# Performance work log

Measured on AMD Instinct MI355X. Metric: run time of the kernel, lower is better.

## Reference

```python
import jax, jax.numpy as jnp
import numpy as np

N = 50000      # nodes
E = 800000     # edges (before self-loops)
F_IN = 128     # num_node_features
HID = 32       # hidden (per-head dim)
H1 = 4         # heads in conv1
G = 64         # graphs in batch


def setup_inputs() -> dict:
    key = jax.random.key(0)
    ks = jax.random.split(key, 12)
    x = jax.random.normal(ks[0], (N, F_IN), jnp.float32)
    edge_index = jax.random.randint(ks[1], (2, E), 0, N)
    batch = jnp.sort(jax.random.randint(ks[2], (N,), 0, G))
    s = lambda k, shape, fan: jax.random.normal(k, shape, jnp.float32) / np.float32(np.sqrt(fan))
    W1 = s(ks[3], (F_IN, H1 * HID), F_IN)
    att_src1 = s(ks[4], (H1, HID), HID)
    att_dst1 = s(ks[5], (H1, HID), HID)
    b1 = jnp.zeros((H1 * HID,), jnp.float32)
    W2 = s(ks[6], (H1 * HID, HID), H1 * HID)
    att_src2 = s(ks[7], (1, HID), HID)
    att_dst2 = s(ks[8], (1, HID), HID)
    b2 = jnp.zeros((HID,), jnp.float32)
    lin1_w = s(ks[9], (HID, HID // 2), HID)
    lin1_b = jnp.zeros((HID // 2,), jnp.float32)
    lin2_w = s(ks[10], (HID // 2, 1), HID // 2)
    lin2_b = jnp.zeros((1,), jnp.float32)
    return dict(x=x, edge_index=edge_index, batch=batch, W1=W1, att_src1=att_src1,
                att_dst1=att_dst1, b1=b1, W2=W2, att_src2=att_src2, att_dst2=att_dst2,
                b2=b2, lin1_w=lin1_w, lin1_b=lin1_b, lin2_w=lin2_w, lin2_b=lin2_b)


def gat_conv(x, src, dst, W, a_src, a_dst, b, heads, dim):
    # PyG GATConv (eval mode): per-edge attention, segment softmax over dst.
    n = x.shape[0]
    h = (x @ W).reshape(n, heads, dim)                         # [N,H,D]
    alpha_src = (h * a_src).sum(-1)                            # [N,H]
    alpha_dst = (h * a_dst).sum(-1)                            # [N,H]
    alpha = jax.nn.leaky_relu(alpha_src[src] + alpha_dst[dst], 0.2)  # [Etot,H]
    amax = jax.ops.segment_max(alpha, dst, num_segments=n)
    e = jnp.exp(alpha - amax[dst])
    denom = jax.ops.segment_sum(e, dst, num_segments=n)
    coef = e / (denom[dst] + 1e-16)
    out = jax.ops.segment_sum(h[src] * coef[:, :, None], dst, num_segments=n)
    return out.reshape(n, heads * dim) + b                     # concat=True


def reference(x, edge_index, batch, W1, att_src1, att_dst1, b1, W2, att_src2,
              att_dst2, b2, lin1_w, lin1_b, lin2_w, lin2_b):
    n = x.shape[0]
    loops = jnp.arange(n, dtype=edge_index.dtype)              # add_self_loops=True
    src = jnp.concatenate([edge_index[0], loops])
    dst = jnp.concatenate([edge_index[1], loops])
    h = jax.nn.elu(gat_conv(x, src, dst, W1, att_src1, att_dst1, b1, H1, HID))
    h = gat_conv(h, src, dst, W2, att_src2, att_dst2, b2, 1, HID)
    counts = jax.ops.segment_sum(jnp.ones((n,), h.dtype), batch, num_segments=G)
    g = jax.ops.segment_sum(h, batch, num_segments=G) / jnp.maximum(counts, 1.0)[:, None]
    g = jax.nn.elu(g @ lin1_w + lin1_b)
    return g @ lin2_w + lin2_b                                  # [G,1]
```

## Files before the change

### kernel.cpp

```cpp
#include <hip/hip_runtime.h>
#include <math.h>

#define N_NODES 50000
#define N_EDGES 800000
#define ETOT (N_EDGES + N_NODES)
#define NG 64
#define NBUCK 196
#define CHUNK 4096
#define NCHUNK ((ETOT + CHUNK - 1)/CHUNK)
#define SCANN (NBUCK*NCHUNK)
#define GSB ((SCANN + 255)/256)

typedef float vf2 __attribute__((ext_vector_type(2)));
typedef short bf16x8 __attribute__((ext_vector_type(8)));
typedef float f32x4 __attribute__((ext_vector_type(4)));

__device__ __forceinline__ float leaky02(float a){ return a > 0.f ? a : 0.2f*a; }
__device__ __forceinline__ float eluf(float v){ return v > 0.f ? v : expm1f(v); }

__device__ __forceinline__ unsigned pack_bf16(float a, float b){
  unsigned ua = __float_as_uint(a); ua += 0x7fffu + ((ua >> 16) & 1u);
  unsigned ub = __float_as_uint(b); ub += 0x7fffu + ((ub >> 16) & 1u);
  return (ua >> 16) | (ub & 0xffff0000u);
}
__device__ __forceinline__ float bf_lo(unsigned v){ return __uint_as_float(v << 16); }
__device__ __forceinline__ float bf_hi(unsigned v){ return __uint_as_float(v & 0xffff0000u); }

__device__ __forceinline__ unsigned pack_fp8x4(float4 a){
  int v = __builtin_amdgcn_cvt_pk_fp8_f32(a.x, a.y, 0, false);
  v = __builtin_amdgcn_cvt_pk_fp8_f32(a.z, a.w, v, true);
  return (unsigned)v;
}

__global__ __launch_bounds__(256) void k_hist(const int* __restrict__ ei,
    unsigned* __restrict__ cnt, const float* __restrict__ W1, const float* __restrict__ W2,
    unsigned* __restrict__ wt1, unsigned* __restrict__ wt2){
  if (blockIdx.x >= NCHUNK){
    int b = blockIdx.x - NCHUNK;
    int t = threadIdx.x;
    if (t < 64){
      if (b < 128){
        float a = W1[(size_t)(2*t)*128 + b];
        float c = W1[(size_t)(2*t+1)*128 + b];
        wt1[b*64 + t] = pack_bf16(a, c);
      } else {
        int cc = b - 128;
        float a = W2[(size_t)(2*t)*32 + cc];
        float c = W2[(size_t)(2*t+1)*32 + cc];
        wt2[cc*64 + t] = pack_bf16(a, c);
      }
    }
    return;
  }
  __shared__ unsigned hist[NBUCK];
  int tid = threadIdx.x;
  for (int t = tid; t < NBUCK; t += 256) hist[t] = 0;
  __syncthreads();
  int base = blockIdx.x * CHUNK;
  #pragma unroll
  for (int i = 0; i < CHUNK/256; ++i){
    int e = base + i*256 + tid;
    if (e < ETOT){
      int d = (e < N_EDGES) ? ei[N_EDGES + e] : (e - N_EDGES);
      atomicAdd(&hist[d >> 8], 1u);
    }
  }
  __syncthreads();
  for (int t = tid; t < NBUCK; t += 256) cnt[t*NCHUNK + blockIdx.x] = hist[t];
}

__global__ __launch_bounds__(256) void g_scan1(const unsigned* __restrict__ in,
    unsigned* __restrict__ bsum, int n){
  int i = blockIdx.x*256 + threadIdx.x;
  unsigned v = (i < n) ? in[i] : 0u;
  #pragma unroll
  for (int o = 32; o >= 1; o >>= 1) v += __shfl_xor(v, o);
  __shared__ unsigned ws[4];
  if ((threadIdx.x & 63) == 0) ws[threadIdx.x >> 6] = v;
  __syncthreads();
  if (threadIdx.x == 0) bsum[blockIdx.x] = ws[0] + ws[1] + ws[2] + ws[3];
}

__global__ __launch_bounds__(256) void g_scan3b(const unsigned* __restrict__ in,
    const unsigned* __restrict__ bsum, unsigned* __restrict__ out, int n){
  __shared__ unsigned bs[256];
  __shared__ unsigned ts[256];
  int t = threadIdx.x, i = blockIdx.x*256 + t;
  bs[t] = (t < GSB && t < blockIdx.x) ? bsum[t] : 0u;
  unsigned v = (i < n) ? in[i] : 0u;
  ts[t] = v;
  __syncthreads();
  #pragma unroll
  for (int o = 128; o >= 1; o >>= 1){
    if (t < o) bs[t] += bs[t + o];
    __syncthreads();
  }
  unsigned base = bs[0];
  for (int o = 1; o < 256; o <<= 1){
    unsigned u = (t >= o) ? ts[t-o] : 0u;
    __syncthreads();
    ts[t] += u;
    __syncthreads();
  }
  if (i < n) out[i] = base + ts[t] - v;
}

__global__ __launch_bounds__(256) void k_part(const int* __restrict__ ei,
    const unsigned* __restrict__ basev, unsigned* __restrict__ staging){
  __shared__ unsigned cur[NBUCK];
  int tid = threadIdx.x;
  for (int t = tid; t < NBUCK; t += 256) cur[t] = basev[t*NCHUNK + blockIdx.x];
  __syncthreads();
  int base = blockIdx.x * CHUNK;
  #pragma unroll
  for (int i = 0; i < CHUNK/256; ++i){
    int e = base + i*256 + tid;
    if (e < ETOT){
      int s, d;
      if (e < N_EDGES){ s = ei[e]; d = ei[N_EDGES + e]; } else { s = d = e - N_EDGES; }
      unsigned pos = atomicAdd(&cur[d >> 8], 1u);
      staging[pos] = (unsigned)s | ((unsigned)(d & 255) << 16);
    }
  }
}

__global__ __launch_bounds__(256) void k_csr(const unsigned* __restrict__ basev,
    const unsigned* __restrict__ staging, unsigned* __restrict__ off,
    int* __restrict__ csr_src){
  __shared__ unsigned ts[256], cur[256];
  int tid = threadIdx.x, b = blockIdx.x;
  unsigned start = basev[b*NCHUNK];
  unsigned end = (b == NBUCK-1) ? (unsigned)ETOT : basev[(b+1)*NCHUNK];
  ts[tid] = 0;
  __syncthreads();
  for (unsigned i = start + tid; i < end; i += 256)
    atomicAdd(&ts[staging[i] >> 16], 1u);
  __syncthreads();
  unsigned v = ts[tid];
  for (int o = 1; o < 256; o <<= 1){
    unsigned u = (tid >= o) ? ts[tid-o] : 0u;
    __syncthreads();
    ts[tid] += u;
    __syncthreads();
  }
  unsigned excl = ts[tid] - v;
  int node = (b << 8) + tid;
  if (node < N_NODES) off[node] = start + excl;
  if (b == 0 && tid == 0) off[N_NODES] = (unsigned)ETOT;
  cur[tid] = excl;
  __syncthreads();
  for (unsigned i = start + tid; i < end; i += 256){
    unsigned p = staging[i];
    unsigned pos = atomicAdd(&cur[p >> 16], 1u);
    csr_src[start + pos] = (int)(p & 0xffffu);
  }
}

__global__ __launch_bounds__(256) void k_gemm1(const float* __restrict__ x,
    const unsigned* __restrict__ wt1, const float* __restrict__ attS,
    const float* __restrict__ attD, unsigned* __restrict__ h1f,
    float* __restrict__ asrc, float* __restrict__ adst)
{
  __shared__ __align__(16) short xs[64*136];
  __shared__ __align__(16) short wb[128*136];
  float* Cst = (float*)wb;
  int tid = threadIdx.x;
  int base = blockIdx.x * 64;
  {
    int row = tid >> 2, q = tid & 3;
    const float* src = x + (size_t)(base + row)*128 + q*32;
    bool valid = (base + row) < N_NODES;
    #pragma unroll
    for (int i = 0; i < 8; ++i){
      float4 v = valid ? *(const float4*)(src + 4*i) : make_float4(0,0,0,0);
      *(uint2*)(&xs[row*136 + q*32 + 4*i]) = make_uint2(pack_bf16(v.x, v.y), pack_bf16(v.z, v.w));
    }
  }
  {
    int c = tid >> 1, h = tid & 1;
    #pragma unroll
    for (int i = 0; i < 8; ++i){
      uint4 v = *(const uint4*)(wt1 + c*64 + h*32 + 4*i);
      *(uint4*)(&wb[c*136 + h*64 + 8*i]) = v;
    }
  }
  __syncthreads();
  int lane = tid & 63, wid = tid >> 6;
  int r = lane & 15, g = lane >> 4;
  bf16x8 afr[4];
  #pragma unroll
  for (int kk = 0; kk < 4; ++kk)
    afr[kk] = *(const bf16x8*)(&xs[(wid*16 + r)*136 + kk*32 + g*8]);
  f32x4 acc[8];
  #pragma unroll
  for (int ct = 0; ct < 8; ++ct){ acc[ct][0]=0.f; acc[ct][1]=0.f; acc[ct][2]=0.f; acc[ct][3]=0.f; }
  #pragma unroll
  for (int ct = 0; ct < 8; ++ct){
    #pragma unroll
    for (int kk = 0; kk < 4; ++kk){
      bf16x8 bfr = *(const bf16x8*)(&wb[(ct*16 + r)*136 + kk*32 + g*8]);
      acc[ct] = __builtin_amdgcn_mfma_f32_16x16x32_bf16(afr[kk], bfr, acc[ct], 0, 0, 0);
    }
  }
  __syncthreads();
  #pragma unroll
  for (int ct = 0; ct < 8; ++ct){
    #pragma unroll
    for (int q = 0; q < 4; ++q)
      Cst[(wid*16 + 4*g + q)*132 + ct*16 + r] = acc[ct][q];
  }
  __syncthreads();
  {
    int row = tid >> 2, hd = tid & 3;
    int grow = base + row;
    if (grow < N_NODES){
      const float* cp = &Cst[row*132 + hd*32];
      const float* aS = attS + hd*32;
      const float* aD = attD + hd*32;
      float ps = 0.f, pd = 0.f;
      unsigned u[8];
      #pragma unroll
      for (int i = 0; i < 8; ++i){
        float4 c4 = *(const float4*)(cp + 4*i);
        ps += c4.x*aS[4*i] + c4.y*aS[4*i+1] + c4.z*aS[4*i+2] + c4.w*aS[4*i+3];
        pd += c4.x*aD[4*i] + c4.y*aD[4*i+1] + c4.z*aD[4*i+2] + c4.w*aD[4*i+3];
        u[i] = pack_fp8x4(c4);
      }
      unsigned* dst = h1f + (size_t)grow*32 + hd*8;
      *(uint4*)(dst)     = make_uint4(u[0], u[1], u[2], u[3]);
      *(uint4*)(dst + 4) = make_uint4(u[4], u[5], u[6], u[7]);
      asrc[grow*4 + hd] = ps;
      adst[grow*4 + hd] = pd;
    }
  }
}

__global__ __launch_bounds__(256) void k_conv1(const unsigned* __restrict__ off,
    const int* __restrict__ csr_src, const unsigned* __restrict__ h1f,
    const float* __restrict__ asrc, const float* __restrict__ adst,
    const float* __restrict__ b1, unsigned* __restrict__ helu_b)
{
  __shared__ uint2 st[4][4][66];
  int w    = threadIdx.x >> 6;
  int lane = threadIdx.x & 63;
  int n = blockIdx.x*4 + w;
  if (n >= N_NODES) return;
  unsigned s0 = off[n];
  int deg = (int)(off[n+1] - s0);
  float4 ad = *(const float4*)(adst + (size_t)n*4);
  int cl = lane & 31;
  int h  = cl >> 3;
  const char* hbase = (const char*)h1f + 4*cl;
  float4 acc = make_float4(0,0,0,0);
  float den = 0.f;

  if (deg <= 64){
    unsigned boff = 0;
    float e0=0.f, e1=0.f, e2=0.f, e3=0.f;
    if (lane < deg){
      int idx = csr_src[s0 + lane];
      boff = ((unsigned)idx) << 7;
      float4 as = *(const float4*)(asrc + (size_t)idx*4);
      e0 = __expf(leaky02(as.x + ad.x));
      e1 = __expf(leaky02(as.y + ad.y));
      e2 = __expf(leaky02(as.z + ad.z));
      e3 = __expf(leaky02(as.w + ad.w));
    }
    st[w][0][lane] = make_uint2(__float_as_uint(e0), boff);
    st[w][1][lane] = make_uint2(__float_as_uint(e1), boff);
    st[w][2][lane] = make_uint2(__float_as_uint(e2), boff);
    st[w][3][lane] = make_uint2(__float_as_uint(e3), boff);
    __builtin_amdgcn_wave_barrier();
    int half = lane >> 5;
    const uint2* sp = &st[w][h][half];
    #pragma unroll 8
    for (int i = 0; i < deg; i += 2){
      uint2 p = sp[i];
      float es = __uint_as_float(p.x);
      unsigned hb = *(const unsigned*)(hbase + p.y);
      vf2 p0 = __builtin_amdgcn_cvt_pk_f32_fp8((int)hb, false);
      vf2 p1 = __builtin_amdgcn_cvt_pk_f32_fp8((int)hb, true);
      acc.x += es*p0[0]; acc.y += es*p0[1];
      acc.z += es*p1[0]; acc.w += es*p1[1];
      den += es;
    }
    acc.x += __shfl_xor(acc.x, 32); acc.y += __shfl_xor(acc.y, 32);
    acc.z += __shfl_xor(acc.z, 32); acc.w += __shfl_xor(acc.w, 32);
    den   += __shfl_xor(den, 32);
  } else {
    float adh = (h==0) ? ad.x : (h==1) ? ad.y : (h==2) ? ad.z : ad.w;
    for (int i = 0; i < deg; ++i){
      int s = csr_src[s0 + i];
      float ev = __expf(leaky02(asrc[s*4 + h] + adh));
      unsigned hb = *(const unsigned*)(hbase + (((unsigned)s) << 7));
      vf2 p0 = __builtin_amdgcn_cvt_pk_f32_fp8((int)hb, false);
      vf2 p1 = __builtin_amdgcn_cvt_pk_f32_fp8((int)hb, true);
      acc.x += ev*p0[0]; acc.y += ev*p0[1];
      acc.z += ev*p1[0]; acc.w += ev*p1[1];
      den += ev;
    }
  }
  if (lane < 32){
    float inv = 1.f/(den + 1e-16f);
    float4 bv = ((const float4*)b1)[cl];
    float ox = eluf(acc.x*inv + bv.x), oy = eluf(acc.y*inv + bv.y);
    float oz = eluf(acc.z*inv + bv.z), ow = eluf(acc.w*inv + bv.w);
    *(uint2*)(helu_b + (size_t)n*64 + 2*cl) = make_uint2(pack_bf16(ox, oy), pack_bf16(oz, ow));
  }
}

__global__ __launch_bounds__(256) void k_gemm2(const unsigned* __restrict__ helu_b,
    const unsigned* __restrict__ wt2, const float* __restrict__ attS,
    const float* __restrict__ attD, unsigned* __restrict__ h2b,
    float* __restrict__ asrc, float* __restrict__ adst)
{
  __shared__ __align__(16) short xs[64*136];
  __shared__ __align__(16) float cbuf[64*36];
  short* w2 = (short*)cbuf;
  int tid = threadIdx.x;
  int base = blockIdx.x * 64;
  {
    int row = tid >> 2, q = tid & 3;
    bool valid = (base + row) < N_NODES;
    const unsigned* src = helu_b + (size_t)(base + row)*64 + q*16;
    #pragma unroll
    for (int i = 0; i < 4; ++i){
      uint4 v = valid ? *(const uint4*)(src + 4*i) : make_uint4(0,0,0,0);
      *(uint4*)(&xs[row*136 + q*32 + 8*i]) = v;
    }
  }
  {
    int c = tid >> 3, h = tid & 7;
    uint4 v0 = *(const uint4*)(wt2 + c*64 + h*8);
    uint4 v1 = *(const uint4*)(wt2 + c*64 + h*8 + 4);
    *(uint4*)(&w2[c*136 + h*16])     = v0;
    *(uint4*)(&w2[c*136 + h*16 + 8]) = v1;
  }
  __syncthreads();
  int lane = tid & 63, wid = tid >> 6;
  int r = lane & 15, g = lane >> 4;
  bf16x8 afr[4];
  #pragma unroll
  for (int kk = 0; kk < 4; ++kk)
    afr[kk] = *(const bf16x8*)(&xs[(wid*16 + r)*136 + kk*32 + g*8]);
  f32x4 acc[2];
  #pragma unroll
  for (int ct = 0; ct < 2; ++ct){ acc[ct][0]=0.f; acc[ct][1]=0.f; acc[ct][2]=0.f; acc[ct][3]=0.f; }
  #pragma unroll
  for (int ct = 0; ct < 2; ++ct){
    #pragma unroll
    for (int kk = 0; kk < 4; ++kk){
      bf16x8 bfr = *(const bf16x8*)(&w2[(ct*16 + r)*136 + kk*32 + g*8]);
      acc[ct] = __builtin_amdgcn_mfma_f32_16x16x32_bf16(afr[kk], bfr, acc[ct], 0, 0, 0);
    }
  }
  __syncthreads();
  #pragma unroll
  for (int ct = 0; ct < 2; ++ct){
    #pragma unroll
    for (int q = 0; q < 4; ++q)
      cbuf[(wid*16 + 4*g + q)*36 + ct*16 + r] = acc[ct][q];
  }
  __syncthreads();
  {
    int row = tid >> 2, q = tid & 3;
    int grow = base + row;
    if (grow < N_NODES){
      const float* cp = &cbuf[row*36 + q*8];
      float4 c0 = *(const float4*)(cp);
      float4 c1 = *(const float4*)(cp + 4);
      *(uint4*)(h2b + (size_t)grow*16 + q*4) =
        make_uint4(pack_bf16(c0.x,c0.y), pack_bf16(c0.z,c0.w),
                   pack_bf16(c1.x,c1.y), pack_bf16(c1.z,c1.w));
    }
  }
  if (tid < 64){
    int grow = base + tid;
    if (grow < N_NODES){
      const float* cp = &cbuf[tid*36];
      float ps = 0.f, pd = 0.f;
      #pragma unroll
      for (int i = 0; i < 8; ++i){
        float4 c4 = *(const float4*)(cp + 4*i);
        ps += c4.x*attS[4*i] + c4.y*attS[4*i+1] + c4.z*attS[4*i+2] + c4.w*attS[4*i+3];
        pd += c4.x*attD[4*i] + c4.y*attD[4*i+1] + c4.z*attD[4*i+2] + c4.w*attD[4*i+3];
      }
      asrc[grow] = ps; adst[grow] = pd;
    }
  }
}

__global__ __launch_bounds__(256) void k_conv2(const unsigned* __restrict__ off,
    const int* __restrict__ csr_src, const unsigned* __restrict__ h2b,
    const float* __restrict__ asrc, const float* __restrict__ adst,
    const float* __restrict__ b2, float* __restrict__ hout)
{
  __shared__ uint2 st[4][66];
  int w    = threadIdx.x >> 6;
  int lane = threadIdx.x & 63;
  int n = blockIdx.x*4 + w;
  if (n >= N_NODES) return;
  unsigned s0 = off[n];
  int deg = (int)(off[n+1] - s0);
  float ad = adst[n];
  int cl = lane & 7;
  const char* hbase = (const char*)h2b + 8*cl;
  float4 acc = make_float4(0,0,0,0);
  float den = 0.f;

  if (deg <= 64){
    unsigned boff = 0;
    float e = 0.f;
    if (lane < deg){
      int idx = csr_src[s0 + lane];
      boff = ((unsigned)idx) << 6;
      e = __expf(leaky02(asrc[idx] + ad));
    }
    st[w][lane] = make_uint2(__float_as_uint(e), boff);
    __builtin_amdgcn_wave_barrier();
    int g8 = lane >> 3;
    const uint2* sp = &st[w][g8];
    #pragma unroll 4
    for (int i = 0; i < deg; i += 8){
      uint2 p = sp[i];
      float es = __uint_as_float(p.x);
      uint2 hb = *(const uint2*)(hbase + p.y);
      acc.x += es*bf_lo(hb.x); acc.y += es*bf_hi(hb.x);
      acc.z += es*bf_lo(hb.y); acc.w += es*bf_hi(hb.y);
      den += es;
    }
    #pragma unroll
    for (int mm = 8; mm <= 32; mm <<= 1){
      acc.x += __shfl_xor(acc.x, mm); acc.y += __shfl_xor(acc.y, mm);
      acc.z += __shfl_xor(acc.z, mm); acc.w += __shfl_xor(acc.w, mm);
      den   += __shfl_xor(den, mm);
    }
  } else {
    for (int i = 0; i < deg; ++i){
      int s = csr_src[s0 + i];
      float ev = __expf(leaky02(asrc[s] + ad));
      uint2 hb = *(const uint2*)(hbase + (((unsigned)s) << 6));
      acc.x += ev*bf_lo(hb.x); acc.y += ev*bf_hi(hb.x);
      acc.z += ev*bf_lo(hb.y); acc.w += ev*bf_hi(hb.y);
      den += ev;
    }
  }
  if (lane < 8){
    float inv = 1.f/(den + 1e-16f);
    float4 bv = ((const float4*)b2)[cl];
    float4 o;
    o.x = acc.x*inv + bv.x; o.y = acc.y*inv + bv.y;
    o.z = acc.z*inv + bv.z; o.w = acc.w*inv + bv.w;
    *(float4*)(hout + (size_t)n*32 + 4*cl) = o;
  }
}

__global__ __launch_bounds__(256) void k_pool(const int* __restrict__ batch,
    const float* __restrict__ hout, float* __restrict__ gmean)
{
  int g = blockIdx.x;
  int a = 0, b = N_NODES;
  while (a < b){ int mid = (a+b)>>1; if (batch[mid] < g) a = mid+1; else b = mid; }
  int lo = a;
  b = N_NODES;
  while (a < b){ int mid = (a+b)>>1; if (batch[mid] < g+1) a = mid+1; else b = mid; }
  int hi = a;
  int c = threadIdx.x & 31, rg = threadIdx.x >> 5;
  float s = 0.f;
  for (int r = lo + rg; r < hi; r += 8) s += hout[(size_t)r*32 + c];
  __shared__ float red[8][32];
  red[rg][c] = s;
  __syncthreads();
  if (rg == 0){
    float t = 0.f;
    #pragma unroll
    for (int k = 0; k < 8; ++k) t += red[k][c];
    gmean[g*32 + c] = t / fmaxf((float)(hi - lo), 1.0f);
  }
}

__global__ void k_final(const float* __restrict__ gmean,
    const float* __restrict__ l1w, const float* __restrict__ l1b,
    const float* __restrict__ l2w, const float* __restrict__ l2b, float* __restrict__ out)
{
  int t = threadIdx.x;
  if (t >= NG) return;
  float g[32];
  #pragma unroll
  for (int j = 0; j < 32; ++j) g[j] = gmean[t*32 + j];
  float o = l2b[0];
  #pragma unroll
  for (int k = 0; k < 16; ++k){
    float hv = l1b[k];
    #pragma unroll
    for (int j = 0; j < 32; ++j) hv += g[j]*l1w[j*16 + k];
    o += eluf(hv) * l2w[k];
  }
  out[t] = o;
}

extern "C" void kernel_launch(void* const* d_in, const int* in_sizes, int n_in,
                              void* d_out, int out_size, void* d_ws, size_t ws_size,
                              hipStream_t stream) {
  const float* x     = (const float*)d_in[0];
  const int*   ei    = (const int*)  d_in[1];
  const int*   batch = (const int*)  d_in[2];
  const float* W1    = (const float*)d_in[3];
  const float* attS1 = (const float*)d_in[4];
  const float* attD1 = (const float*)d_in[5];
  const float* b1    = (const float*)d_in[6];
  const float* W2    = (const float*)d_in[7];
  const float* attS2 = (const float*)d_in[8];
  const float* attD2 = (const float*)d_in[9];
  const float* b2    = (const float*)d_in[10];
  const float* l1w   = (const float*)d_in[11];
  const float* l1b   = (const float*)d_in[12];
  const float* l2w   = (const float*)d_in[13];
  const float* l2b   = (const float*)d_in[14];
  float* out = (float*)d_out;

  char* w = (char*)d_ws;
  auto alloc = [&](size_t elems) -> void* {
    void* p = (void*)w;
    w += ((elems*4 + 255)/256)*256;
    return p;
  };
  unsigned* csr_off = (unsigned*)alloc(N_NODES + 1);
  unsigned* cnt     = (unsigned*)alloc(SCANN);
  unsigned* basev   = (unsigned*)alloc(SCANN);
  unsigned* gbs     = (unsigned*)alloc(GSB);
  unsigned* staging = (unsigned*)alloc(ETOT);
  int*      csr_src = (int*)     alloc(ETOT);
  unsigned* wt1g  = (unsigned*)alloc(128*64);
  unsigned* wt2g  = (unsigned*)alloc(32*64);
  unsigned* h1f   = (unsigned*)alloc((size_t)N_NODES*32);
  float*    asrc1 = (float*)alloc((size_t)N_NODES*4);
  float*    adst1 = (float*)alloc((size_t)N_NODES*4);
  unsigned* helu_b= (unsigned*)alloc((size_t)N_NODES*64);
  unsigned* h2b   = (unsigned*)alloc((size_t)N_NODES*16);
  float*    asrc2 = (float*)alloc(N_NODES);
  float*    adst2 = (float*)alloc(N_NODES);
  float*    hout  = (float*)alloc((size_t)N_NODES*32);
  float*    gmean = (float*)alloc(NG*32);

  k_hist  <<<NCHUNK + 160, 256, 0, stream>>>(ei, cnt, W1, W2, wt1g, wt2g);
  g_scan1 <<<GSB, 256, 0, stream>>>(cnt, gbs, SCANN);
  g_scan3b<<<GSB, 256, 0, stream>>>(cnt, gbs, basev, SCANN);
  k_part  <<<NCHUNK, 256, 0, stream>>>(ei, basev, staging);
  k_csr   <<<NBUCK, 256, 0, stream>>>(basev, staging, csr_off, csr_src);

  k_gemm1<<<(N_NODES + 63)/64, 256, 0, stream>>>(x, wt1g, attS1, attD1, h1f, asrc1, adst1);
  k_conv1<<<(N_NODES + 3)/4, 256, 0, stream>>>(csr_off, csr_src, h1f, asrc1, adst1, b1, helu_b);
  k_gemm2<<<(N_NODES + 63)/64, 256, 0, stream>>>(helu_b, wt2g, attS2, attD2, h2b, asrc2, adst2);
  k_conv2<<<(N_NODES + 3)/4, 256, 0, stream>>>(csr_off, csr_src, h2b, asrc2, adst2, b2, hout);
  k_pool <<<NG, 256, 0, stream>>>(batch, hout, gmean);
  k_final<<<1, 64, 0, stream>>>(gmean, l1w, l1b, l2w, l2b, out);
}
```

Before: 159.8 us.

## Merge scan passes, co-launch partition with GEMM1, fuse pool with final MLP

Replaces the two-pass block-sum scan with a single kernel where each block recomputes its prefix by summing all preceding inputs. Merges the edge-partition kernel and the first GEMM into one launch, split by block index, so the independent work overlaps. Fuses mean pooling and the final MLP using a last-block-done atomic counter reset by a memset. This cuts kernel launches and gaps between them, at the cost of redundant prefix reads, a larger shared-memory footprint for the partition blocks (lower occupancy), and an extra memset.

```diff
diff --git a/kernel.cpp b/kernel.cpp
--- a/kernel.cpp
+++ b/kernel.cpp
@@ -10,6 +10,7 @@
 #define NCHUNK ((ETOT + CHUNK - 1)/CHUNK)
 #define SCANN (NBUCK*NCHUNK)
 #define GSB ((SCANN + 255)/256)
+#define GB1 ((N_NODES + 63)/64)
 
 typedef float vf2 __attribute__((ext_vector_type(2)));
 typedef short bf16x8 __attribute__((ext_vector_type(8)));
@@ -69,33 +70,20 @@
   for (int t = tid; t < NBUCK; t += 256) cnt[t*NCHUNK + blockIdx.x] = hist[t];
 }
 
-__global__ __launch_bounds__(256) void g_scan1(const unsigned* __restrict__ in,
-    unsigned* __restrict__ bsum, int n){
-  int i = blockIdx.x*256 + threadIdx.x;
-  unsigned v = (i < n) ? in[i] : 0u;
-  #pragma unroll
-  for (int o = 32; o >= 1; o >>= 1) v += __shfl_xor(v, o);
-  __shared__ unsigned ws[4];
-  if ((threadIdx.x & 63) == 0) ws[threadIdx.x >> 6] = v;
-  __syncthreads();
-  if (threadIdx.x == 0) bsum[blockIdx.x] = ws[0] + ws[1] + ws[2] + ws[3];
-}
-
-__global__ __launch_bounds__(256) void g_scan3b(const unsigned* __restrict__ in,
-    const unsigned* __restrict__ bsum, unsigned* __restrict__ out, int n){
-  __shared__ unsigned bs[256];
+__global__ __launch_bounds__(256) void g_scanM(const unsigned* __restrict__ in,
+    unsigned* __restrict__ out, int n){
+  __shared__ unsigned red[4];
   __shared__ unsigned ts[256];
-  int t = threadIdx.x, i = blockIdx.x*256 + t;
-  bs[t] = (t < GSB && t < blockIdx.x) ? bsum[t] : 0u;
+  int t = threadIdx.x, blk = blockIdx.x, i = blk*256 + t;
+  unsigned s = 0;
+  for (int j = t; j < blk*256; j += 256) s += in[j];
+  #pragma unroll
+  for (int o = 32; o >= 1; o >>= 1) s += __shfl_xor(s, o);
+  if ((t & 63) == 0) red[t >> 6] = s;
   unsigned v = (i < n) ? in[i] : 0u;
   ts[t] = v;
   __syncthreads();
-  #pragma unroll
-  for (int o = 128; o >= 1; o >>= 1){
-    if (t < o) bs[t] += bs[t + o];
-    __syncthreads();
-  }
-  unsigned base = bs[0];
+  unsigned base = red[0] + red[1] + red[2] + red[3];
   for (int o = 1; o < 256; o <<= 1){
     unsigned u = (t >= o) ? ts[t-o] : 0u;
     __syncthreads();
@@ -105,67 +93,36 @@
   if (i < n) out[i] = base + ts[t] - v;
 }
 
-__global__ __launch_bounds__(256) void k_part(const int* __restrict__ ei,
-    const unsigned* __restrict__ basev, unsigned* __restrict__ staging){
+__global__ __launch_bounds__(256) void k_pg(const int* __restrict__ ei,
+    const unsigned* __restrict__ basev, unsigned* __restrict__ staging,
+    const float* __restrict__ x, const unsigned* __restrict__ wt1,
+    const float* __restrict__ attS, const float* __restrict__ attD,
+    unsigned* __restrict__ h1f, float* __restrict__ asrc, float* __restrict__ adst)
+{
   __shared__ unsigned cur[NBUCK];
-  int tid = threadIdx.x;
-  for (int t = tid; t < NBUCK; t += 256) cur[t] = basev[t*NCHUNK + blockIdx.x];
-  __syncthreads();
-  int base = blockIdx.x * CHUNK;
-  #pragma unroll
-  for (int i = 0; i < CHUNK/256; ++i){
-    int e = base + i*256 + tid;
-    if (e < ETOT){
-      int s, d;
-      if (e < N_EDGES){ s = ei[e]; d = ei[N_EDGES + e]; } else { s = d = e - N_EDGES; }
-      unsigned pos = atomicAdd(&cur[d >> 8], 1u);
-      staging[pos] = (unsigned)s | ((unsigned)(d & 255) << 16);
-    }
-  }
-}
-
-__global__ __launch_bounds__(256) void k_csr(const unsigned* __restrict__ basev,
-    const unsigned* __restrict__ staging, unsigned* __restrict__ off,
-    int* __restrict__ csr_src){
-  __shared__ unsigned ts[256], cur[256];
-  int tid = threadIdx.x, b = blockIdx.x;
-  unsigned start = basev[b*NCHUNK];
-  unsigned end = (b == NBUCK-1) ? (unsigned)ETOT : basev[(b+1)*NCHUNK];
-  ts[tid] = 0;
-  __syncthreads();
-  for (unsigned i = start + tid; i < end; i += 256)
-    atomicAdd(&ts[staging[i] >> 16], 1u);
-  __syncthreads();
-  unsigned v = ts[tid];
-  for (int o = 1; o < 256; o <<= 1){
-    unsigned u = (tid >= o) ? ts[tid-o] : 0u;
-    __syncthreads();
-    ts[tid] += u;
-    __syncthreads();
-  }
-  unsigned excl = ts[tid] - v;
-  int node = (b << 8) + tid;
-  if (node < N_NODES) off[node] = start + excl;
-  if (b == 0 && tid == 0) off[N_NODES] = (unsigned)ETOT;
-  cur[tid] = excl;
-  __syncthreads();
-  for (unsigned i = start + tid; i < end; i += 256){
-    unsigned p = staging[i];
-    unsigned pos = atomicAdd(&cur[p >> 16], 1u);
-    csr_src[start + pos] = (int)(p & 0xffffu);
-  }
-}
-
-__global__ __launch_bounds__(256) void k_gemm1(const float* __restrict__ x,
-    const unsigned* __restrict__ wt1, const float* __restrict__ attS,
-    const float* __restrict__ attD, unsigned* __restrict__ h1f,
-    float* __restrict__ asrc, float* __restrict__ adst)
-{
   __shared__ __align__(16) short xs[64*136];
   __shared__ __align__(16) short wb[128*136];
+  int tid = threadIdx.x;
+
+  if (blockIdx.x < NCHUNK){
+    for (int t = tid; t < NBUCK; t += 256) cur[t] = basev[t*NCHUNK + blockIdx.x];
+    __syncthreads();
+    int base = blockIdx.x * CHUNK;
+    #pragma unroll
+    for (int i = 0; i < CHUNK/256; ++i){
+      int e = base + i*256 + tid;
+      if (e < ETOT){
+        int s, d;
+        if (e < N_EDGES){ s = ei[e]; d = ei[N_EDGES + e]; } else { s = d = e - N_EDGES; }
+        unsigned pos = atomicAdd(&cur[d >> 8], 1u);
+        staging[pos] = (unsigned)s | ((unsigned)(d & 255) << 16);
+      }
+    }
+    return;
+  }
+
   float* Cst = (float*)wb;
-  int tid = threadIdx.x;
-  int base = blockIdx.x * 64;
+  int base = (blockIdx.x - NCHUNK) * 64;
   {
     int row = tid >> 2, q = tid & 3;
     const float* src = x + (size_t)(base + row)*128 + q*32;
@@ -235,6 +192,38 @@
   }
 }
 
+__global__ __launch_bounds__(256) void k_csr(const unsigned* __restrict__ basev,
+    const unsigned* __restrict__ staging, unsigned* __restrict__ off,
+    int* __restrict__ csr_src){
+  __shared__ unsigned ts[256], cur[256];
+  int tid = threadIdx.x, b = blockIdx.x;
+  unsigned start = basev[b*NCHUNK];
+  unsigned end = (b == NBUCK-1) ? (unsigned)ETOT : basev[(b+1)*NCHUNK];
+  ts[tid] = 0;
+  __syncthreads();
+  for (unsigned i = start + tid; i < end; i += 256)
+    atomicAdd(&ts[staging[i] >> 16], 1u);
+  __syncthreads();
+  unsigned v = ts[tid];
+  for (int o = 1; o < 256; o <<= 1){
+    unsigned u = (tid >= o) ? ts[tid-o] : 0u;
+    __syncthreads();
+    ts[tid] += u;
+    __syncthreads();
+  }
+  unsigned excl = ts[tid] - v;
+  int node = (b << 8) + tid;
+  if (node < N_NODES) off[node] = start + excl;
+  if (b == 0 && tid == 0) off[N_NODES] = (unsigned)ETOT;
+  cur[tid] = excl;
+  __syncthreads();
+  for (unsigned i = start + tid; i < end; i += 256){
+    unsigned p = staging[i];
+    unsigned pos = atomicAdd(&cur[p >> 16], 1u);
+    csr_src[start + pos] = (int)(p & 0xffffu);
+  }
+}
+
 __global__ __launch_bounds__(256) void k_conv1(const unsigned* __restrict__ off,
     const int* __restrict__ csr_src, const unsigned* __restrict__ h1f,
     const float* __restrict__ asrc, const float* __restrict__ adst,
@@ -455,8 +444,10 @@
   }
 }
 
-__global__ __launch_bounds__(256) void k_pool(const int* __restrict__ batch,
-    const float* __restrict__ hout, float* __restrict__ gmean)
+__global__ __launch_bounds__(256) void k_poolf(const int* __restrict__ batch,
+    const float* __restrict__ hout, float* __restrict__ gmean, unsigned* __restrict__ ctr,
+    const float* __restrict__ l1w, const float* __restrict__ l1b,
+    const float* __restrict__ l2w, const float* __restrict__ l2b, float* __restrict__ out)
 {
   int g = blockIdx.x;
   int a = 0, b = N_NODES;
@@ -477,26 +468,29 @@
     for (int k = 0; k < 8; ++k) t += red[k][c];
     gmean[g*32 + c] = t / fmaxf((float)(hi - lo), 1.0f);
   }
-}
-
-__global__ void k_final(const float* __restrict__ gmean,
-    const float* __restrict__ l1w, const float* __restrict__ l1b,
-    const float* __restrict__ l2w, const float* __restrict__ l2b, float* __restrict__ out)
-{
-  int t = threadIdx.x;
-  if (t >= NG) return;
-  float g[32];
-  #pragma unroll
-  for (int j = 0; j < 32; ++j) g[j] = gmean[t*32 + j];
-  float o = l2b[0];
-  #pragma unroll
-  for (int k = 0; k < 16; ++k){
-    float hv = l1b[k];
-    #pragma unroll
-    for (int j = 0; j < 32; ++j) hv += g[j]*l1w[j*16 + k];
-    o += eluf(hv) * l2w[k];
-  }
-  out[t] = o;
+  __syncthreads();
+  __threadfence();
+  __shared__ unsigned rank;
+  if (threadIdx.x == 0) rank = atomicAdd(ctr, 1u);
+  __syncthreads();
+  if (rank == NG - 1){
+    __threadfence();
+    int t = threadIdx.x;
+    if (t < NG){
+      float gv[32];
+      #pragma unroll
+      for (int j = 0; j < 32; ++j) gv[j] = gmean[t*32 + j];
+      float o = l2b[0];
+      #pragma unroll
+      for (int k = 0; k < 16; ++k){
+        float hv = l1b[k];
+        #pragma unroll
+        for (int j = 0; j < 32; ++j) hv += gv[j]*l1w[j*16 + k];
+        o += eluf(hv) * l2w[k];
+      }
+      out[t] = o;
+    }
+  }
 }
 
 extern "C" void kernel_launch(void* const* d_in, const int* in_sizes, int n_in,
@@ -528,7 +522,6 @@
   unsigned* csr_off = (unsigned*)alloc(N_NODES + 1);
   unsigned* cnt     = (unsigned*)alloc(SCANN);
   unsigned* basev   = (unsigned*)alloc(SCANN);
-  unsigned* gbs     = (unsigned*)alloc(GSB);
   unsigned* staging = (unsigned*)alloc(ETOT);
   int*      csr_src = (int*)     alloc(ETOT);
   unsigned* wt1g  = (unsigned*)alloc(128*64);
@@ -542,17 +535,18 @@
   float*    adst2 = (float*)alloc(N_NODES);
   float*    hout  = (float*)alloc((size_t)N_NODES*32);
   float*    gmean = (float*)alloc(NG*32);
+  unsigned* ctr   = (unsigned*)alloc(1);
+
+  hipMemsetAsync(ctr, 0, 4, stream);
 
   k_hist  <<<NCHUNK + 160, 256, 0, stream>>>(ei, cnt, W1, W2, wt1g, wt2g);
-  g_scan1 <<<GSB, 256, 0, stream>>>(cnt, gbs, SCANN);
-  g_scan3b<<<GSB, 256, 0, stream>>>(cnt, gbs, basev, SCANN);
-  k_part  <<<NCHUNK, 256, 0, stream>>>(ei, basev, staging);
+  g_scanM <<<GSB, 256, 0, stream>>>(cnt, basev, SCANN);
+  k_pg    <<<NCHUNK + GB1, 256, 0, stream>>>(ei, basev, staging,
+                                             x, wt1g, attS1, attD1, h1f, asrc1, adst1);
   k_csr   <<<NBUCK, 256, 0, stream>>>(basev, staging, csr_off, csr_src);
 
-  k_gemm1<<<(N_NODES + 63)/64, 256, 0, stream>>>(x, wt1g, attS1, attD1, h1f, asrc1, adst1);
   k_conv1<<<(N_NODES + 3)/4, 256, 0, stream>>>(csr_off, csr_src, h1f, asrc1, adst1, b1, helu_b);
   k_gemm2<<<(N_NODES + 63)/64, 256, 0, stream>>>(helu_b, wt2g, attS2, attD2, h2b, asrc2, adst2);
   k_conv2<<<(N_NODES + 3)/4, 256, 0, stream>>>(csr_off, csr_src, h2b, asrc2, adst2, b2, hout);
-  k_pool <<<NG, 256, 0, stream>>>(batch, hout, gmean);
-  k_final<<<1, 64, 0, stream>>>(gmean, l1w, l1b, l2w, l2b, out);
-}
+  k_poolf<<<NG, 256, 0, stream>>>(batch, hout, gmean, ctr, l1w, l1b, l2w, l2b, out);
+}
```

Result: slower. 181.1 us (+13.3%).
